# Performance work log

Measured on AMD Instinct MI355X. Metric: run time of the kernel, lower is better.

The kernel has to match this reference:

```python
import jax, jax.numpy as jnp
from jax import lax
import numpy as np

BN_EPS = 1e-5
LN_EPS = 1e-5


def _ln(x, g, b):
    m = x.mean(-1, keepdims=True)
    v = ((x - m) ** 2).mean(-1, keepdims=True)
    return (x - m) / jnp.sqrt(v + LN_EPS) * g + b


def _bn(x, g, b):
    # eval-mode BatchNorm2d with running_mean=0, running_var=1
    s = g / np.float32(np.sqrt(1.0 + BN_EPS))
    return x * s[None, :, None, None] + b[None, :, None, None]


def _conv(x, w, b, pad=0):
    y = lax.conv_general_dilated(x, w, (1, 1), [(pad, pad), (pad, pad)],
                                 dimension_numbers=('NCHW', 'OIHW', 'NCHW'))
    return y + b[None, :, None, None]


def _t2p(t, H, W):  # token2patch: [B,N,C] -> [B,C,H,W]
    B, N, C = t.shape
    return t.transpose(0, 2, 1).reshape(B, C, H, W)


def _p2t(x):  # patch2token: [B,C,H,W] -> [B,H*W,C]
    B, C, H, W = x.shape
    return x.reshape(B, C, H * W).transpose(0, 2, 1)


def _sgn(x, cw, cr_w, cr_b, ci_w, ci_b, g1, b1, g2, b2):
    # SpectralGatingNetwork. x: [B,C,H,W]; torch permute(0,3,2,1) -> [B,W,H,C]
    xp = x.transpose(0, 3, 2, 1)
    f = jnp.fft.rfft2(xp, axes=(1, 2), norm='ortho')  # [B,W,H//2+1,C]
    fr = jax.nn.relu(_bn(_conv(f.real.transpose(0, 3, 1, 2), cr_w, cr_b), g1, b1))
    fi = jax.nn.relu(_bn(_conv(f.imag.transpose(0, 3, 1, 2), ci_w, ci_b), g2, b2))
    fc = (fr + 1j * fi).transpose(0, 2, 3, 1) * (cw[..., 0] + 1j * cw[..., 1])
    out = jnp.fft.irfft2(fc, s=(xp.shape[1], xp.shape[2]), axes=(1, 2), norm='ortho')
    return out.transpose(0, 3, 2, 1)


def _forward(p):
    x = p['x']
    B, N, D = x.shape
    # ---- Attention_Module (self.sum) ----
    y = jax.nn.relu(x @ p['am_lin_w'] + p['am_lin_b'])  # [B,N,8]
    H, dh = 8, 1  # Attention(8, num_heads=8) -> head_dim 1, scale 1
    qkv = (y @ p['am_qkv_w'] + p['am_qkv_b']).reshape(B, N, 3, H, dh).transpose(2, 0, 3, 1, 4)
    q, k, v = qkv[0], qkv[1], qkv[2]
    attn = jax.nn.softmax(jnp.einsum('bhnd,bhmd->bhnm', q, k) * (dh ** -0.5), axis=-1)
    av = jnp.einsum('bhnm,bhmd->bhnd', attn, v).transpose(0, 2, 1, 3).reshape(B, N, 8)
    av = av @ p['am_proj_w'] + p['am_proj_b']
    x0 = _ln(x + (y + av) @ p['am_end_w'] + p['am_end_b'], p['am_ln_g'], p['am_ln_b'])
    # ---- mlp2(norm2(x0)), timm Mlp hidden=dim, exact GELU ----
    h = _ln(x0, p['ln2_g'], p['ln2_b'])
    x0 = jax.nn.gelu(h @ p['mlp_fc1_w'] + p['mlp_fc1_b'], approximate=False) @ p['mlp_fc2_w'] + p['mlp_fc2_b']
    # ---- adapter branch ----
    xa = x @ p['ad_w'] + p['ad_b']  # [B,320,8]
    z = _t2p(xa[:, :64], 8, 8)      # template tokens -> 8x8
    xr = _t2p(xa[:, 64:], 16, 16)   # search tokens -> 16x16
    # search-region branch
    x1 = jax.nn.relu(_bn(_conv(xr, p['b1_w'], p['b1_b']), p['b1_bn_g'], p['b1_bn_b']))
    xo = _sgn(x1, p['sx_cw'], p['sx_cr_w'], p['sx_cr_b'], p['sx_ci_w'], p['sx_ci_b'],
              p['sx_bn1_g'], p['sx_bn1_b'], p['sx_bn2_g'], p['sx_bn2_b']) + x1
    xo = _bn(_conv(xo, p['c1_w'], p['c1_b']), p['bn_g'], p['bn_b'])
    xo = jax.nn.relu(_p2t(xo))
    x2 = _conv(xr, p['c3_w'], p['c3_b'], pad=1)
    xo = _bn(_t2p(xo, 16, 16) + x2, p['bn_g'], p['bn_b'])
    xo = jax.nn.relu(_p2t(xo))
    # template branch
    z1 = jax.nn.relu(_bn(_conv(z, p['b2_w'], p['b2_b']), p['b2_bn_g'], p['b2_bn_b']))
    zo = _sgn(z1, p['sz_cw'], p['sz_cr_w'], p['sz_cr_b'], p['sz_ci_w'], p['sz_ci_b'],
              p['sz_bn1_g'], p['sz_bn1_b'], p['sz_bn2_g'], p['sz_bn2_b']) + z1
    zo = _bn(_conv(zo, p['c2_w'], p['c2_b']), p['bn_g'], p['bn_b'])
    zo = jax.nn.relu(_p2t(zo))
    z2 = _conv(z, p['c4_w'], p['c4_b'], pad=1)
    zo = _bn(_t2p(zo, 8, 8) + z2, p['bn_g'], p['bn_b'])
    zo = jax.nn.relu(_p2t(zo))
    xf = jnp.concatenate([zo, xo], axis=1) @ p['au_w'] + p['au_b']
    return xf + x0


def setup_inputs() -> dict:
    key = jax.random.key(0)
    ki = iter(jax.random.split(key, 64))
    def rn(shape, s=0.02):
        return jax.random.normal(next(ki), shape, dtype=jnp.float32) * s
    z8 = jnp.zeros((8,), jnp.float32)
    o8 = jnp.ones((8,), jnp.float32)
    z768 = jnp.zeros((768,), jnp.float32)
    o768 = jnp.ones((768,), jnp.float32)
    inp = dict(
        x=jax.random.normal(next(ki), (128, 320, 768), jnp.float32),
        am_lin_w=rn((768, 8)), am_lin_b=z8,
        am_qkv_w=rn((8, 24)), am_qkv_b=jnp.zeros((24,), jnp.float32),
        am_proj_w=rn((8, 8)), am_proj_b=z8,
        am_end_w=rn((8, 768)), am_end_b=z768,
        am_ln_g=o768, am_ln_b=z768,
        ln2_g=o768, ln2_b=z768,
        mlp_fc1_w=rn((768, 768)), mlp_fc1_b=z768,
        mlp_fc2_w=rn((768, 768)), mlp_fc2_b=z768,
        ad_w=rn((768, 8)), ad_b=z8,
        au_w=rn((8, 768)), au_b=z768,
        b1_w=rn((8, 8, 1, 1)), b1_b=z8, b1_bn_g=o8, b1_bn_b=z8,
        b2_w=rn((8, 8, 1, 1)), b2_b=z8, b2_bn_g=o8, b2_bn_b=z8,
        sx_cw=rn((16, 9, 8, 2)), sx_cr_w=rn((8, 8, 1, 1)), sx_cr_b=z8,
        sx_ci_w=rn((8, 8, 1, 1)), sx_ci_b=z8,
        sx_bn1_g=o8, sx_bn1_b=z8, sx_bn2_g=o8, sx_bn2_b=z8,
        sz_cw=rn((8, 5, 8, 2)), sz_cr_w=rn((8, 8, 1, 1)), sz_cr_b=z8,
        sz_ci_w=rn((8, 8, 1, 1)), sz_ci_b=z8,
        sz_bn1_g=o8, sz_bn1_b=z8, sz_bn2_g=o8, sz_bn2_b=z8,
        c1_w=rn((8, 8, 1, 1)), c1_b=z8, c2_w=rn((8, 8, 1, 1)), c2_b=z8,
        c3_w=rn((8, 8, 3, 3)), c3_b=z8, c4_w=rn((8, 8, 3, 3)), c4_b=z8,
        bn_g=o8, bn_b=z8,
    )
    return inp


def reference(x, am_lin_w, am_lin_b, am_qkv_w, am_qkv_b, am_proj_w, am_proj_b,
              am_end_w, am_end_b, am_ln_g, am_ln_b, ln2_g, ln2_b,
              mlp_fc1_w, mlp_fc1_b, mlp_fc2_w, mlp_fc2_b,
              ad_w, ad_b, au_w, au_b,
              b1_w, b1_b, b1_bn_g, b1_bn_b, b2_w, b2_b, b2_bn_g, b2_bn_b,
              sx_cw, sx_cr_w, sx_cr_b, sx_ci_w, sx_ci_b,
              sx_bn1_g, sx_bn1_b, sx_bn2_g, sx_bn2_b,
              sz_cw, sz_cr_w, sz_cr_b, sz_ci_w, sz_ci_b,
              sz_bn1_g, sz_bn1_b, sz_bn2_g, sz_bn2_b,
              c1_w, c1_b, c2_w, c2_b, c3_w, c3_b, c4_w, c4_b, bn_g, bn_b):
    return _forward(dict(locals()))
```

## Files before the change

kernel.cpp:

```cpp
#include <hip/hip_runtime.h>
#include <hip/hip_bf16.h>

typedef unsigned short u16;
typedef __bf16 bf16x8 __attribute__((ext_vector_type(8)));
typedef float f32x4 __attribute__((ext_vector_type(4)));

#define B_    128
#define N_TOK 320
#define D_    768
#define M_TOT (B_ * N_TOK)

__device__ __forceinline__ u16 f2b(float x) {
  __hip_bfloat16 t = __float2bfloat16(x);
  return *reinterpret_cast<u16*>(&t);
}

typedef const __attribute__((address_space(1))) void* gas1_t;
typedef __attribute__((address_space(3))) void* las3_t;
__device__ __forceinline__ void gll16(const void* g, void* l) {
  __builtin_amdgcn_global_load_lds((gas1_t)g, (las3_t)l, 16, 0, 0);
}

__device__ __forceinline__ void block_reduce2(float& a, float& b, float* red, int t) {
  #pragma unroll
  for (int off = 32; off >= 1; off >>= 1) {
    a += __shfl_xor(a, off);
    b += __shfl_xor(b, off);
  }
  int wv = t >> 6;
  __syncthreads();
  if ((t & 63) == 0) { red[wv] = a; red[4 + wv] = b; }
  __syncthreads();
  a = red[0] + red[1] + red[2] + red[3];
  b = red[4] + red[5] + red[6] + red[7];
}

__global__ __launch_bounds__(256) void k_transpose_bf16(const float* __restrict__ in,
                                                        u16* __restrict__ out) {
  __shared__ float tile[32][33];
  int c0 = blockIdx.x * 32, r0 = blockIdx.y * 32;
  int tx = threadIdx.x, ty = threadIdx.y;
  #pragma unroll
  for (int k = 0; k < 4; k++)
    tile[ty + k * 8][tx] = in[(size_t)(r0 + ty + k * 8) * 768 + c0 + tx];
  __syncthreads();
  #pragma unroll
  for (int k = 0; k < 4; k++)
    out[(size_t)(c0 + ty + k * 8) * 768 + r0 + tx] = f2b(tile[tx][ty + k * 8]);
}

__global__ __launch_bounds__(256) void k_token_a(
    const float* __restrict__ x,
    const float* __restrict__ lin_w, const float* __restrict__ lin_b,
    const float* __restrict__ qkv_w, const float* __restrict__ qkv_b,
    const float* __restrict__ ad_w, const float* __restrict__ ad_b,
    float* __restrict__ y_out, float* __restrict__ xa_out,
    float* __restrict__ q_out, float* __restrict__ k_out, float* __restrict__ v_out) {
  __shared__ __align__(16) float w_lds[16 * 768];
  int t = threadIdx.x;
  for (int i = t; i < 6144; i += 256) {
    w_lds[(i & 7) * 768 + (i >> 3)] = lin_w[i];
    w_lds[((i & 7) + 8) * 768 + (i >> 3)] = ad_w[i];
  }
  __syncthreads();
  int wave = t >> 6, lane = t & 63;
  for (int it = 0; it < 10; ++it) {
    int tok = blockIdx.x * 4 + wave + it * 4096;
    const float* xr = x + (size_t)tok * 768;
    float p[16];
    #pragma unroll
    for (int j = 0; j < 16; j++) p[j] = 0.f;
    #pragma unroll
    for (int u = 0; u < 3; u++) {
      float4 xv = *reinterpret_cast<const float4*>(xr + u * 256 + lane * 4);
      #pragma unroll
      for (int j = 0; j < 16; j++) {
        float4 wv = *reinterpret_cast<const float4*>(&w_lds[j * 768 + u * 256 + lane * 4]);
        p[j] += xv.x * wv.x + xv.y * wv.y + xv.z * wv.z + xv.w * wv.w;
      }
    }
    #pragma unroll
    for (int j = 0; j < 16; j++) {
      #pragma unroll
      for (int off = 32; off >= 1; off >>= 1) p[j] += __shfl_xor(p[j], off);
    }
    float yv[8];
    #pragma unroll
    for (int j = 0; j < 8; j++) yv[j] = fmaxf(p[j] + lin_b[j], 0.f);
    if (lane == 0) {
      #pragma unroll
      for (int j = 0; j < 8; j++) {
        y_out[(size_t)tok * 8 + j] = yv[j];
        xa_out[(size_t)tok * 8 + j] = p[8 + j] + ad_b[j];
      }
    }
    if (lane < 24) {
      float o = qkv_b[lane];
      #pragma unroll
      for (int j = 0; j < 8; j++) o += yv[j] * qkv_w[j * 24 + lane];
      int b = tok / 320, n = tok % 320;
      int hh = lane & 7;
      size_t idx = ((size_t)b * 8 + hh) * 320 + n;
      if (lane < 8) q_out[idx] = o;
      else if (lane < 16) k_out[idx] = o;
      else v_out[idx] = o;
    }
  }
}

__global__ __launch_bounds__(320) void k_attn(
    const float* __restrict__ q, const float* __restrict__ k,
    const float* __restrict__ v, float* __restrict__ av) {
  __shared__ float ks[320], vs[320];
  __shared__ float red[12];
  int bh = blockIdx.x;
  int n = threadIdx.x;
  float kk = k[(size_t)bh * 320 + n];
  ks[n] = kk;
  vs[n] = v[(size_t)bh * 320 + n];
  float qn = q[(size_t)bh * 320 + n];
  float mx = kk, mn = kk;
  #pragma unroll
  for (int off = 32; off >= 1; off >>= 1) {
    mx = fmaxf(mx, __shfl_xor(mx, off));
    mn = fminf(mn, __shfl_xor(mn, off));
  }
  int wave = n >> 6;
  if ((n & 63) == 0) { red[wave] = mx; red[5 + wave] = mn; }
  __syncthreads();
  if (n == 0) {
    float a = red[0], b = red[5];
    #pragma unroll
    for (int w = 1; w < 5; w++) { a = fmaxf(a, red[w]); b = fminf(b, red[5 + w]); }
    red[10] = a; red[11] = b;
  }
  __syncthreads();
  float kmax = red[10], kmin = red[11];
  float m1 = fmaxf(qn * kmax, qn * kmin);
  float se = 0.f, sv = 0.f;
  for (int m = 0; m < 320; m++) {
    float e = __expf(qn * ks[m] - m1);
    se += e;
    sv += e * vs[m];
  }
  int b_ = bh >> 3, h_ = bh & 7;
  av[(((size_t)b_ * 320) + n) * 8 + h_] = sv / se;
}

__global__ __launch_bounds__(256) void k_token_c(
    const float* __restrict__ x, const float* __restrict__ y_ws, const float* __restrict__ av_ws,
    const float* __restrict__ proj_w, const float* __restrict__ proj_b,
    const float* __restrict__ end_w, const float* __restrict__ end_b,
    const float* __restrict__ g1ln, const float* __restrict__ b1ln,
    const float* __restrict__ g2ln, const float* __restrict__ b2ln,
    u16* __restrict__ hout) {
  __shared__ float red[8];
  size_t tok = blockIdx.x;
  int t = threadIdx.x;
  float u[8];
  #pragma unroll
  for (int o = 0; o < 8; o++) {
    float a = proj_b[o];
    #pragma unroll
    for (int j = 0; j < 8; j++) a += av_ws[tok * 8 + j] * proj_w[j * 8 + o];
    u[o] = a + y_ws[tok * 8 + o];
  }
  float tv[3];
  #pragma unroll
  for (int c = 0; c < 3; c++) {
    int d = t + c * 256;
    float a = x[tok * 768 + d] + end_b[d];
    #pragma unroll
    for (int j = 0; j < 8; j++) a += u[j] * end_w[j * 768 + d];
    tv[c] = a;
  }
  float s = tv[0] + tv[1] + tv[2];
  float s2 = tv[0] * tv[0] + tv[1] * tv[1] + tv[2] * tv[2];
  block_reduce2(s, s2, red, t);
  float m1 = s * (1.f / 768.f);
  float inv1 = rsqrtf(fmaxf(s2 * (1.f / 768.f) - m1 * m1, 0.f) + 1e-5f);
  float x0[3];
  #pragma unroll
  for (int c = 0; c < 3; c++) {
    int d = t + c * 256;
    x0[c] = (tv[c] - m1) * inv1 * g1ln[d] + b1ln[d];
  }
  s = x0[0] + x0[1] + x0[2];
  s2 = x0[0] * x0[0] + x0[1] * x0[1] + x0[2] * x0[2];
  block_reduce2(s, s2, red, t);
  float m2 = s * (1.f / 768.f);
  float inv2 = rsqrtf(fmaxf(s2 * (1.f / 768.f) - m2 * m2, 0.f) + 1e-5f);
  #pragma unroll
  for (int c = 0; c < 3; c++) {
    int d = t + c * 256;
    float hv = (x0[c] - m2) * inv2 * g2ln[d] + b2ln[d];
    hout[tok * 768 + d] = f2b(hv);
  }
}

template <int S>
__global__ __launch_bounds__(256) void k_adapter(
    const float* __restrict__ xa,
    const float* __restrict__ bw, const float* __restrict__ bb,
    const float* __restrict__ bng0, const float* __restrict__ bnb0,
    const float* __restrict__ cw,
    const float* __restrict__ crw, const float* __restrict__ crb,
    const float* __restrict__ ciw, const float* __restrict__ cib,
    const float* __restrict__ bn1g, const float* __restrict__ bn1b,
    const float* __restrict__ bn2g, const float* __restrict__ bn2b,
    const float* __restrict__ cvw, const float* __restrict__ cvb,
    const float* __restrict__ c3w, const float* __restrict__ c3b,
    const float* __restrict__ bng, const float* __restrict__ bnb,
    float* __restrict__ crout, int tok_off) {
  constexpr int NF = S / 2 + 1;
  constexpr int P = S * S;
  constexpr int NFREQ = S * NF * 8;
  __shared__ float xr[8 * P];
  __shared__ float x1[8 * P];
  __shared__ float xo[8 * P];
  __shared__ float bufA[NFREQ * 2];
  __shared__ float bufB[NFREQ * 2];
  __shared__ float cosT[S], sinT[S];
  const int b = blockIdx.x, t = threadIdx.x;
  const float binv = rsqrtf(1.f + 1e-5f);
  if (t < S) {
    float ang = 6.28318530717958647692f * (float)t / (float)S;
    cosT[t] = cosf(ang);
    sinT[t] = sinf(ang);
  }
  for (int i = t; i < 8 * P; i += 256) {
    int c = i / P, p = i % P;
    xr[i] = xa[((size_t)b * N_TOK + tok_off + p) * 8 + c];
  }
  __syncthreads();
  for (int i = t; i < 8 * P; i += 256) {
    int c = i / P, p = i % P;
    float a = bb[c];
    #pragma unroll
    for (int j = 0; j < 8; j++) a += xr[j * P + p] * bw[c * 8 + j];
    a = a * (bng0[c] * binv) + bnb0[c];
    x1[i] = fmaxf(a, 0.f);
  }
  __syncthreads();
  for (int i = t; i < NFREQ; i += 256) {
    int c = i & 7, v = (i >> 3) % NF, w = i / (8 * NF);
    float re = 0.f, im = 0.f;
    #pragma unroll
    for (int h = 0; h < S; h++) {
      float xv = x1[c * P + h * S + w];
      int idx = (v * h) % S;
      re += xv * cosT[idx];
      im -= xv * sinT[idx];
    }
    bufA[i * 2] = re;
    bufA[i * 2 + 1] = im;
  }
  __syncthreads();
  for (int i = t; i < NFREQ; i += 256) {
    int c = i & 7, v = (i >> 3) % NF, u = i / (8 * NF);
    float re = 0.f, im = 0.f;
    #pragma unroll
    for (int w = 0; w < S; w++) {
      float ar = bufA[((w * NF + v) * 8 + c) * 2];
      float ai = bufA[((w * NF + v) * 8 + c) * 2 + 1];
      int idx = (u * w) % S;
      float cs = cosT[idx], sn = sinT[idx];
      re += ar * cs + ai * sn;
      im += ai * cs - ar * sn;
    }
    bufB[i * 2] = re * (1.f / S);
    bufB[i * 2 + 1] = im * (1.f / S);
  }
  __syncthreads();
  for (int i = t; i < NFREQ; i += 256) {
    int c = i & 7;
    int uv = i >> 3;
    float fr = crb[c], fi = cib[c];
    #pragma unroll
    for (int j = 0; j < 8; j++) {
      fr += bufB[(uv * 8 + j) * 2] * crw[c * 8 + j];
      fi += bufB[(uv * 8 + j) * 2 + 1] * ciw[c * 8 + j];
    }
    fr = fmaxf(fr * (bn1g[c] * binv) + bn1b[c], 0.f);
    fi = fmaxf(fi * (bn2g[c] * binv) + bn2b[c], 0.f);
    float cwr = cw[i * 2], cwi = cw[i * 2 + 1];
    bufA[i * 2] = fr * cwr - fi * cwi;
    bufA[i * 2 + 1] = fr * cwi + fi * cwr;
  }
  __syncthreads();
  for (int i = t; i < NFREQ; i += 256) {
    int c = i & 7, v = (i >> 3) % NF, w = i / (8 * NF);
    float re = 0.f, im = 0.f;
    #pragma unroll
    for (int u = 0; u < S; u++) {
      float gr = bufA[((u * NF + v) * 8 + c) * 2];
      float gi = bufA[((u * NF + v) * 8 + c) * 2 + 1];
      int idx = (u * w) % S;
      float cs = cosT[idx], sn = sinT[idx];
      re += gr * cs - gi * sn;
      im += gi * cs + gr * sn;
    }
    bufB[((w * NF + v) * 8 + c) * 2] = re;
    bufB[((w * NF + v) * 8 + c) * 2 + 1] = im;
  }
  __syncthreads();
  for (int i = t; i < 8 * P; i += 256) {
    int c = i / P, p = i % P, h = p / S, w = p % S;
    float acc = bufB[((w * NF + 0) * 8 + c) * 2];
    float ny = bufB[((w * NF + (NF - 1)) * 8 + c) * 2];
    acc += (h & 1) ? -ny : ny;
    #pragma unroll
    for (int v = 1; v < NF - 1; v++) {
      int idx = (v * h) % S;
      acc += 2.f * (bufB[((w * NF + v) * 8 + c) * 2] * cosT[idx] -
                    bufB[((w * NF + v) * 8 + c) * 2 + 1] * sinT[idx]);
    }
    xo[i] = acc * (1.f / S) + x1[i];
  }
  __syncthreads();
  for (int i = t; i < 8 * P; i += 256) {
    int c = i / P, p = i % P, h = p / S, w = p % S;
    float a = cvb[c];
    #pragma unroll
    for (int j = 0; j < 8; j++) a += xo[j * P + p] * cvw[c * 8 + j];
    a = fmaxf(a * (bng[c] * binv) + bnb[c], 0.f);
    float x2 = c3b[c];
    #pragma unroll
    for (int j = 0; j < 8; j++) {
      #pragma unroll
      for (int dy = 0; dy < 3; dy++) {
        int hh = h + dy - 1;
        if (hh < 0 || hh >= S) continue;
        #pragma unroll
        for (int dx = 0; dx < 3; dx++) {
          int ww = w + dx - 1;
          if (ww < 0 || ww >= S) continue;
          x2 += xr[j * P + hh * S + ww] * c3w[((c * 8 + j) * 3 + dy) * 3 + dx];
        }
      }
    }
    float fin = (a + x2) * (bng[c] * binv) + bnb[c];
    crout[((size_t)b * N_TOK + tok_off + p) * 8 + c] = fmaxf(fin, 0.f);
  }
}

template <int MODE>
__global__ __launch_bounds__(256) void k_gemm(
    const u16* __restrict__ A, const u16* __restrict__ Bt,
    const float* __restrict__ bias,
    u16* __restrict__ obf, float* __restrict__ ofp,
    const float* __restrict__ au_w, const float* __restrict__ au_b,
    const float* __restrict__ cr) {
  __shared__ __align__(16) u16 As[128 * 32];
  __shared__ __align__(16) u16 Bs[128 * 32];
  int bid = blockIdx.x;
  int bm = bid / 6, bn = bid % 6;
  int m0 = bm * 128, n0 = bn * 128;
  int t = threadIdx.x, wave = t >> 6, lane = t & 63;
  int wr = wave >> 1, wc = wave & 1;
  const int l15 = lane & 15, l4 = lane >> 4;
  f32x4 acc[4][4];
  #pragma unroll
  for (int mi = 0; mi < 4; mi++)
    #pragma unroll
    for (int ni = 0; ni < 4; ni++) {
      f32x4 z = {0.f, 0.f, 0.f, 0.f};
      acc[mi][ni] = z;
    }
  for (int k0 = 0; k0 < 768; k0 += 32) {
    #pragma unroll
    for (int i = 0; i < 2; i++) {
      int chunk = i * 256 + t;
      int r = chunk >> 2, kp = (chunk & 3) * 8;
      gll16(A + (size_t)(m0 + r) * 768 + k0 + kp, (void*)&As[(i * 256 + wave * 64) * 8]);
      gll16(Bt + (size_t)(n0 + r) * 768 + k0 + kp, (void*)&Bs[(i * 256 + wave * 64) * 8]);
    }
    __syncthreads();
    bf16x8 af[4], bfr[4];
    #pragma unroll
    for (int mi = 0; mi < 4; mi++)
      af[mi] = *reinterpret_cast<const bf16x8*>(&As[(wr * 64 + mi * 16 + l15) * 32 + l4 * 8]);
    #pragma unroll
    for (int ni = 0; ni < 4; ni++)
      bfr[ni] = *reinterpret_cast<const bf16x8*>(&Bs[(wc * 64 + ni * 16 + l15) * 32 + l4 * 8]);
    #pragma unroll
    for (int mi = 0; mi < 4; mi++)
      #pragma unroll
      for (int ni = 0; ni < 4; ni++)
        acc[mi][ni] = __builtin_amdgcn_mfma_f32_16x16x32_bf16(af[mi], bfr[ni], acc[mi][ni], 0, 0, 0);
    __syncthreads();
  }
  #pragma unroll
  for (int mi = 0; mi < 4; mi++) {
    #pragma unroll
    for (int ni = 0; ni < 4; ni++) {
      int colg = n0 + wc * 64 + ni * 16 + l15;
      #pragma unroll
      for (int rg = 0; rg < 4; rg++) {
        int rowg = m0 + wr * 64 + mi * 16 + l4 * 4 + rg;
        float vv = acc[mi][ni][rg] + bias[colg];
        if constexpr (MODE == 1) {
          vv = 0.5f * vv * (1.f + erff(vv * 0.70710678118654752f));
          obf[(size_t)rowg * 768 + colg] = f2b(vv);
        } else {
          vv += au_b[colg];
          const float* crr = cr + (size_t)rowg * 8;
          #pragma unroll
          for (int j = 0; j < 8; j++) vv += crr[j] * au_w[j * 768 + colg];
          ofp[(size_t)rowg * 768 + colg] = vv;
        }
      }
    }
  }
}

extern "C" void kernel_launch(void* const* d_in, const int* in_sizes, int n_in,
                              void* d_out, int out_size, void* d_ws, size_t ws_size,
                              hipStream_t stream) {
  const float* x        = (const float*)d_in[0];
  const float* am_lin_w = (const float*)d_in[1];
  const float* am_lin_b = (const float*)d_in[2];
  const float* am_qkv_w = (const float*)d_in[3];
  const float* am_qkv_b = (const float*)d_in[4];
  const float* am_proj_w= (const float*)d_in[5];
  const float* am_proj_b= (const float*)d_in[6];
  const float* am_end_w = (const float*)d_in[7];
  const float* am_end_b = (const float*)d_in[8];
  const float* am_ln_g  = (const float*)d_in[9];
  const float* am_ln_b  = (const float*)d_in[10];
  const float* ln2_g    = (const float*)d_in[11];
  const float* ln2_b    = (const float*)d_in[12];
  const float* fc1_w    = (const float*)d_in[13];
  const float* fc1_b    = (const float*)d_in[14];
  const float* fc2_w    = (const float*)d_in[15];
  const float* fc2_b    = (const float*)d_in[16];
  const float* ad_w     = (const float*)d_in[17];
  const float* ad_b     = (const float*)d_in[18];
  const float* au_w     = (const float*)d_in[19];
  const float* au_b     = (const float*)d_in[20];
  const float* b1_w     = (const float*)d_in[21];
  const float* b1_b     = (const float*)d_in[22];
  const float* b1_bn_g  = (const float*)d_in[23];
  const float* b1_bn_b  = (const float*)d_in[24];
  const float* b2_w     = (const float*)d_in[25];
  const float* b2_b     = (const float*)d_in[26];
  const float* b2_bn_g  = (const float*)d_in[27];
  const float* b2_bn_b  = (const float*)d_in[28];
  const float* sx_cw    = (const float*)d_in[29];
  const float* sx_cr_w  = (const float*)d_in[30];
  const float* sx_cr_b  = (const float*)d_in[31];
  const float* sx_ci_w  = (const float*)d_in[32];
  const float* sx_ci_b  = (const float*)d_in[33];
  const float* sx_bn1_g = (const float*)d_in[34];
  const float* sx_bn1_b = (const float*)d_in[35];
  const float* sx_bn2_g = (const float*)d_in[36];
  const float* sx_bn2_b = (const float*)d_in[37];
  const float* sz_cw    = (const float*)d_in[38];
  const float* sz_cr_w  = (const float*)d_in[39];
  const float* sz_cr_b  = (const float*)d_in[40];
  const float* sz_ci_w  = (const float*)d_in[41];
  const float* sz_ci_b  = (const float*)d_in[42];
  const float* sz_bn1_g = (const float*)d_in[43];
  const float* sz_bn1_b = (const float*)d_in[44];
  const float* sz_bn2_g = (const float*)d_in[45];
  const float* sz_bn2_b = (const float*)d_in[46];
  const float* c1_w     = (const float*)d_in[47];
  const float* c1_b     = (const float*)d_in[48];
  const float* c2_w     = (const float*)d_in[49];
  const float* c2_b     = (const float*)d_in[50];
  const float* c3_w     = (const float*)d_in[51];
  const float* c3_b     = (const float*)d_in[52];
  const float* c4_w     = (const float*)d_in[53];
  const float* c4_b     = (const float*)d_in[54];
  const float* bn_g     = (const float*)d_in[55];
  const float* bn_b     = (const float*)d_in[56];

  char* ws = (char*)d_ws;
  constexpr size_t H_OFF   = 0;
  constexpr size_t G1_OFF  = 62914560;
  constexpr size_t W1T_OFF = 125829120;
  constexpr size_t W2T_OFF = W1T_OFF + 1179648;
  constexpr size_t Y_OFF   = W2T_OFF + 1179648;
  constexpr size_t XA_OFF  = Y_OFF + 1310720;
  constexpr size_t AV_OFF  = XA_OFF + 1310720;
  constexpr size_t Q_OFF   = AV_OFF + 1310720;
  constexpr size_t K_OFF   = Q_OFF + 1310720;
  constexpr size_t V_OFF   = K_OFF + 1310720;
  constexpr size_t CR_OFF  = V_OFF + 1310720;

  u16* h_ws   = (u16*)(ws + H_OFF);
  u16* g1_ws  = (u16*)(ws + G1_OFF);
  u16* w1t    = (u16*)(ws + W1T_OFF);
  u16* w2t    = (u16*)(ws + W2T_OFF);
  float* y_ws = (float*)(ws + Y_OFF);
  float* xa_ws= (float*)(ws + XA_OFF);
  float* av_ws= (float*)(ws + AV_OFF);
  float* q_ws = (float*)(ws + Q_OFF);
  float* k_ws = (float*)(ws + K_OFF);
  float* v_ws = (float*)(ws + V_OFF);
  float* cr_ws= (float*)(ws + CR_OFF);

  k_transpose_bf16<<<dim3(24, 24), dim3(32, 8), 0, stream>>>(fc1_w, w1t);
  k_transpose_bf16<<<dim3(24, 24), dim3(32, 8), 0, stream>>>(fc2_w, w2t);
  k_token_a<<<1024, 256, 0, stream>>>(x, am_lin_w, am_lin_b, am_qkv_w, am_qkv_b,
                                      ad_w, ad_b, y_ws, xa_ws, q_ws, k_ws, v_ws);
  k_attn<<<1024, 320, 0, stream>>>(q_ws, k_ws, v_ws, av_ws);
  k_token_c<<<M_TOT, 256, 0, stream>>>(x, y_ws, av_ws, am_proj_w, am_proj_b,
                                       am_end_w, am_end_b, am_ln_g, am_ln_b,
                                       ln2_g, ln2_b, h_ws);
  k_adapter<8><<<128, 256, 0, stream>>>(xa_ws, b2_w, b2_b, b2_bn_g, b2_bn_b, sz_cw,
                                        sz_cr_w, sz_cr_b, sz_ci_w, sz_ci_b,
                                        sz_bn1_g, sz_bn1_b, sz_bn2_g, sz_bn2_b,
                                        c2_w, c2_b, c4_w, c4_b, bn_g, bn_b, cr_ws, 0);
  k_adapter<16><<<128, 256, 0, stream>>>(xa_ws, b1_w, b1_b, b1_bn_g, b1_bn_b, sx_cw,
                                         sx_cr_w, sx_cr_b, sx_ci_w, sx_ci_b,
                                         sx_bn1_g, sx_bn1_b, sx_bn2_g, sx_bn2_b,
                                         c1_w, c1_b, c3_w, c3_b, bn_g, bn_b, cr_ws, 64);
  k_gemm<1><<<1920, 256, 0, stream>>>(h_ws, w1t, fc1_b, g1_ws, nullptr, nullptr, nullptr, nullptr);
  k_gemm<2><<<1920, 256, 0, stream>>>(g1_ws, w2t, fc2_b, nullptr, (float*)d_out, au_w, au_b, cr_ws);
}
```

Measured before the change: 802.9 us.

## Double-buffer GEMM LDS tiles with BK=64, XOR swizzle, and XCD-aware block remap

Reworks the MLP GEMM main loop to use two LDS buffers with a K-tile of 64, issuing the next tile's global-to-LDS loads before computing the current one so memory latency overlaps MFMA work, and halving the number of barriers per K. Adds an XOR swizzle on LDS columns to reduce bank conflicts on the fragment reads. Remaps block IDs so consecutive blocks on an XCD share A/B tiles for better L2 reuse, and sets a minimum of two blocks per CU in the launch bounds. LDS use grows fourfold to 64KB per block, which may limit occupancy. The block remap assumes a grid of exactly 1920 blocks.

After: 716.6 us. 10.7% less time.

```diff
diff --git a/kernel.cpp b/kernel.cpp
--- a/kernel.cpp
+++ b/kernel.cpp
@@ -345,20 +345,34 @@
 }
 
 template <int MODE>
-__global__ __launch_bounds__(256) void k_gemm(
+__global__ __launch_bounds__(256, 2) void k_gemm(
     const u16* __restrict__ A, const u16* __restrict__ Bt,
     const float* __restrict__ bias,
     u16* __restrict__ obf, float* __restrict__ ofp,
     const float* __restrict__ au_w, const float* __restrict__ au_b,
     const float* __restrict__ cr) {
-  __shared__ __align__(16) u16 As[128 * 32];
-  __shared__ __align__(16) u16 Bs[128 * 32];
-  int bid = blockIdx.x;
-  int bm = bid / 6, bn = bid % 6;
+  __shared__ __align__(16) u16 As[2][128 * 64];
+  __shared__ __align__(16) u16 Bs[2][128 * 64];
+  int orig = blockIdx.x;
+  int wgid = (orig & 7) * 240 + (orig >> 3);
+  int bm = wgid / 6, bn = wgid % 6;
   int m0 = bm * 128, n0 = bn * 128;
   int t = threadIdx.x, wave = t >> 6, lane = t & 63;
   int wr = wave >> 1, wc = wave & 1;
   const int l15 = lane & 15, l4 = lane >> 4;
+  const int swz = (l15 & 7) << 4;
+
+  const char* srcA[4];
+  const char* srcB[4];
+  #pragma unroll
+  for (int i = 0; i < 4; i++) {
+    int b = i * 256 + t;
+    int row = b >> 3;
+    int colb = ((b & 7) << 4) ^ ((row & 7) << 4);
+    srcA[i] = (const char*)A + (size_t)(m0 + row) * 1536 + colb;
+    srcB[i] = (const char*)Bt + (size_t)(n0 + row) * 1536 + colb;
+  }
+
   f32x4 acc[4][4];
   #pragma unroll
   for (int mi = 0; mi < 4; mi++)
@@ -367,29 +381,57 @@
       f32x4 z = {0.f, 0.f, 0.f, 0.f};
       acc[mi][ni] = z;
     }
-  for (int k0 = 0; k0 < 768; k0 += 32) {
-    #pragma unroll
-    for (int i = 0; i < 2; i++) {
-      int chunk = i * 256 + t;
-      int r = chunk >> 2, kp = (chunk & 3) * 8;
-      gll16(A + (size_t)(m0 + r) * 768 + k0 + kp, (void*)&As[(i * 256 + wave * 64) * 8]);
-      gll16(Bt + (size_t)(n0 + r) * 768 + k0 + kp, (void*)&Bs[(i * 256 + wave * 64) * 8]);
-    }
+
+  auto STAGE = [&](int buf, int k0) {
+    #pragma unroll
+    for (int i = 0; i < 4; i++) {
+      int basechunk = i * 256 + wave * 64;
+      gll16(srcA[i] + 2 * k0, (void*)&As[buf][basechunk * 8]);
+      gll16(srcB[i] + 2 * k0, (void*)&Bs[buf][basechunk * 8]);
+    }
+  };
+
+  auto COMPUTE = [&](int buf) {
+    const char* abase = (const char*)&As[buf][0];
+    const char* bbase = (const char*)&Bs[buf][0];
+    bf16x8 af[2][4], bf[2][4];
+    #pragma unroll
+    for (int kk = 0; kk < 2; kk++) {
+      int c = kk * 64 + l4 * 16;
+      int cs = c ^ swz;
+      #pragma unroll
+      for (int mi = 0; mi < 4; mi++) {
+        int R = wr * 64 + mi * 16 + l15;
+        af[kk][mi] = *reinterpret_cast<const bf16x8*>(abase + R * 128 + cs);
+      }
+      #pragma unroll
+      for (int ni = 0; ni < 4; ni++) {
+        int R = wc * 64 + ni * 16 + l15;
+        bf[kk][ni] = *reinterpret_cast<const bf16x8*>(bbase + R * 128 + cs);
+      }
+    }
+    #pragma unroll
+    for (int kk = 0; kk < 2; kk++)
+      #pragma unroll
+      for (int mi = 0; mi < 4; mi++)
+        #pragma unroll
+        for (int ni = 0; ni < 4; ni++)
+          acc[mi][ni] = __builtin_amdgcn_mfma_f32_16x16x32_bf16(af[kk][mi], bf[kk][ni],
+                                                                acc[mi][ni], 0, 0, 0);
+  };
+
+  STAGE(0, 0);
+  __syncthreads();
+  int cur = 0;
+  #pragma unroll 1
+  for (int s = 0; s < 11; ++s) {
+    STAGE(cur ^ 1, (s + 1) * 64);
+    COMPUTE(cur);
     __syncthreads();
-    bf16x8 af[4], bfr[4];
-    #pragma unroll
-    for (int mi = 0; mi < 4; mi++)
-      af[mi] = *reinterpret_cast<const bf16x8*>(&As[(wr * 64 + mi * 16 + l15) * 32 + l4 * 8]);
-    #pragma unroll
-    for (int ni = 0; ni < 4; ni++)
-      bfr[ni] = *reinterpret_cast<const bf16x8*>(&Bs[(wc * 64 + ni * 16 + l15) * 32 + l4 * 8]);
-    #pragma unroll
-    for (int mi = 0; mi < 4; mi++)
-      #pragma unroll
-      for (int ni = 0; ni < 4; ni++)
-        acc[mi][ni] = __builtin_amdgcn_mfma_f32_16x16x32_bf16(af[mi], bfr[ni], acc[mi][ni], 0, 0, 0);
-    __syncthreads();
-  }
+    cur ^= 1;
+  }
+  COMPUTE(cur);
+
   #pragma unroll
   for (int mi = 0; mi < 4; mi++) {
     #pragma unroll
```
